# Optimization experiments

Hardware: AMD Instinct MI355X
Metric: run time of the kernel (lower is better)

The kernel has to match this reference:

```python
import jax, jax.numpy as jnp
import numpy as np

ALPHA = 0.7
MARGIN = 0.5
BATCH = 8192


def setup_inputs() -> dict:
    key = jax.random.key(0)
    k1, k2 = jax.random.split(key)
    predictions = jax.random.normal(k1, (BATCH, 1), dtype=jnp.float32)
    targets = jax.random.normal(k2, (BATCH, 1), dtype=jnp.float32)
    return {"predictions": predictions, "targets": targets}


def reference(predictions, targets):
    # MSE term (mean over all elements, as nn.MSELoss default)
    mse_loss = jnp.mean((predictions - targets) ** 2)

    p = predictions[:, 0]  # [B]
    t = targets[:, 0]      # [B]
    B = p.shape[0]

    # Pairwise differences [B, B]
    dt = t[:, None] - t[None, :]
    dp = p[:, None] - p[None, :]

    # Original loop visits ordered pairs i < j and, depending on sign(t_i - t_j),
    # computes relu(margin - sign(t_i - t_j) * (p_i - p_j)); ties are skipped.
    upper = jnp.triu(jnp.ones((B, B), dtype=bool), k=1)
    valid = upper & (dt != 0)
    pair_loss = jax.nn.relu(MARGIN - jnp.sign(dt) * dp)

    count = jnp.sum(valid)
    ranking_sum = jnp.sum(jnp.where(valid, pair_loss, 0.0))
    ranking_loss = jnp.where(count > 0, ranking_sum / jnp.maximum(count, 1), 0.0)

    return ALPHA * mse_loss + (1.0 - ALPHA) * ranking_loss
```

## Files before the change

### kernel.cpp

```cpp
#include <hip/hip_runtime.h>

#define ALPHA  0.7f
#define MARGIN 0.5f
#define TI 64
#define TJ 256
#define JR 4

__global__ __launch_bounds__(64) void pair_kernel(const float* __restrict__ p,
                                                  const float* __restrict__ t,
                                                  int B,
                                                  float* __restrict__ bsum,
                                                  float* __restrict__ bmse,
                                                  int*   __restrict__ bcnt) {
    const int bid = blockIdx.x;
    int jt = (int)((sqrtf(1.0f + 2.0f * (float)bid) - 1.0f) * 0.5f);
    while (2 * (jt + 1) * (jt + 2) <= bid) ++jt;
    while (2 * jt * (jt + 1) > bid) --jt;
    const int it  = bid - 2 * jt * (jt + 1);

    const int tid   = threadIdx.x;
    const int ig0   = it * TI;
    const int jbase = jt * TJ;
    const int j0    = jbase + tid * JR;

    __shared__ float2 s_tp[TI];
    {
        const int ig = ig0 + tid;
        float2 v;
        if (ig < B) { v.x = t[ig]; v.y = p[ig]; }
        else        { v.x = 0.0f;  v.y = 0.0f;  }
        s_tp[tid] = v;
    }
    __syncthreads();

    float tjv[JR], pjv[JR];
    bool  jvb[JR];
    if (j0 + JR <= B) {
        const float4 tv = *reinterpret_cast<const float4*>(t + j0);
        const float4 pv = *reinterpret_cast<const float4*>(p + j0);
        tjv[0] = tv.x; tjv[1] = tv.y; tjv[2] = tv.z; tjv[3] = tv.w;
        pjv[0] = pv.x; pjv[1] = pv.y; pjv[2] = pv.z; pjv[3] = pv.w;
        jvb[0] = jvb[1] = jvb[2] = jvb[3] = true;
    } else {
        #pragma unroll
        for (int k = 0; k < JR; ++k) {
            const int jg = j0 + k;
            jvb[k] = jg < B;
            tjv[k] = jvb[k] ? t[jg] : 0.0f;
            pjv[k] = jvb[k] ? p[jg] : 0.0f;
        }
    }
    unsigned long long jm[JR];
    #pragma unroll
    for (int k = 0; k < JR; ++k) jm[k] = __ballot(jvb[k]);

    float sum[JR] = {0.0f, 0.0f, 0.0f, 0.0f};
    int   cnt = 0;
    float msev = 0.0f;

    if (it == 4 * jt) {
        #pragma unroll
        for (int k = 0; k < JR; ++k) {
            const float d = pjv[k] - tjv[k];
            msev += jvb[k] ? d * d : 0.0f;
        }
    }

    if (it < 4 * jt) {
        #pragma unroll 8
        for (int ii = 0; ii < TI; ++ii) {
            const float2 itp = s_tp[ii];
            #pragma unroll
            for (int k = 0; k < JR; ++k) {
                const float dt = itp.x - tjv[k];
                const float dp = itp.y - pjv[k];
                const unsigned sg = __float_as_uint(dt) & 0x80000000u;
                const float sdp = __uint_as_float(__float_as_uint(dp) ^ sg);
                const float v = fmaxf(MARGIN - sdp, 0.0f);
                const bool val = (dt != 0.0f);
                sum[k] += val ? v : 0.0f;
                cnt += (int)__popcll(__ballot(val) & jm[k]);
            }
        }
    } else {
        int jloc[JR];
        #pragma unroll
        for (int k = 0; k < JR; ++k) jloc[k] = j0 + k - ig0;
        #pragma unroll 4
        for (int ii = 0; ii < TI; ++ii) {
            const float2 itp = s_tp[ii];
            #pragma unroll
            for (int k = 0; k < JR; ++k) {
                const float dt = itp.x - tjv[k];
                const float dp = itp.y - pjv[k];
                const unsigned sg = __float_as_uint(dt) & 0x80000000u;
                const float sdp = __uint_as_float(__float_as_uint(dp) ^ sg);
                const float v = fmaxf(MARGIN - sdp, 0.0f);
                const bool val = (dt != 0.0f) && (ii < jloc[k]);
                sum[k] += val ? v : 0.0f;
                cnt += (int)__popcll(__ballot(val) & jm[k]);
            }
        }
    }

    float stot = 0.0f;
    #pragma unroll
    for (int k = 0; k < JR; ++k) stot += jvb[k] ? sum[k] : 0.0f;
    for (int off = 32; off > 0; off >>= 1) {
        stot += __shfl_down(stot, off);
        msev += __shfl_down(msev, off);
    }
    if (tid == 0) {
        bsum[bid] = stot;
        bmse[bid] = msev;
        bcnt[bid] = cnt;
    }
}

__global__ __launch_bounds__(256) void finalize_kernel(const float* __restrict__ bsum,
                                                       const float* __restrict__ bmse,
                                                       const int*   __restrict__ bcnt,
                                                       int NB, int B,
                                                       float* __restrict__ out) {
    const int tid = threadIdx.x;
    double S = 0.0, M = 0.0;
    long long C = 0;
    for (int k = tid; k < NB; k += 256) {
        S += (double)bsum[k];
        M += (double)bmse[k];
        C += (long long)bcnt[k];
    }
    for (int off = 32; off > 0; off >>= 1) {
        S += __shfl_down(S, off);
        M += __shfl_down(M, off);
        C += __shfl_down(C, off);
    }
    __shared__ double rs[4], rm[4];
    __shared__ long long rc[4];
    const int wid = tid >> 6, lane = tid & 63;
    if (lane == 0) { rs[wid] = S; rm[wid] = M; rc[wid] = C; }
    __syncthreads();
    if (tid == 0) {
        S = rs[0] + rs[1] + rs[2] + rs[3];
        M = rm[0] + rm[1] + rm[2] + rm[3];
        C = rc[0] + rc[1] + rc[2] + rc[3];
        const double mse  = M / (double)B;
        const double rank = (C > 0) ? (S / (double)(C > 1 ? C : 1)) : 0.0;
        out[0] = (float)((double)ALPHA * mse + (double)(1.0f - ALPHA) * rank);
    }
}

extern "C" void kernel_launch(void* const* d_in, const int* in_sizes, int n_in,
                              void* d_out, int out_size, void* d_ws, size_t ws_size,
                              hipStream_t stream) {
    const float* p = (const float*)d_in[0];
    const float* t = (const float*)d_in[1];
    const int B = in_sizes[0];

    const int NJ = (B + TJ - 1) / TJ;
    const int NB = 2 * NJ * (NJ + 1);

    float* bsum = (float*)d_ws;
    float* bmse = bsum + NB;
    int*   bcnt = (int*)(bmse + NB);

    pair_kernel<<<NB, 64, 0, stream>>>(p, t, B, bsum, bmse, bcnt);
    finalize_kernel<<<1, 256, 0, stream>>>(bsum, bmse, bcnt, NB, B, (float*)d_out);
}
```

Before: 22.50 us.

## Count valid pairs analytically and read i-values from global memory with smaller i-tiles

The pair count is no longer built from a per-iteration ballot and popcount. It is computed as the number of in-range pairs minus tie pairs, and the tie correction runs only when a wave detects an equal t via __any. The shared-memory staging and barrier are removed: i-values are read straight from global memory as wave-uniform loads, and the i-tile is halved, which doubles the block count. This cuts per-pair instruction count, but adds more blocks and per-iteration global loads that depend on cache hits.

```diff
diff --git a/kernel.cpp b/kernel.cpp
--- a/kernel.cpp
+++ b/kernel.cpp
@@ -2,9 +2,9 @@
 
 #define ALPHA  0.7f
 #define MARGIN 0.5f
-#define TI 64
-#define TJ 256
-#define JR 4
+#define TI  32
+#define TJN 256
+#define JR  4
 
 __global__ __launch_bounds__(64) void pair_kernel(const float* __restrict__ p,
                                                   const float* __restrict__ t,
@@ -13,25 +13,14 @@
                                                   float* __restrict__ bmse,
                                                   int*   __restrict__ bcnt) {
     const int bid = blockIdx.x;
-    int jt = (int)((sqrtf(1.0f + 2.0f * (float)bid) - 1.0f) * 0.5f);
-    while (2 * (jt + 1) * (jt + 2) <= bid) ++jt;
-    while (2 * jt * (jt + 1) > bid) --jt;
-    const int it  = bid - 2 * jt * (jt + 1);
+    int jt = (int)((sqrtf((float)bid + 1.0f) - 1.0f) * 0.5f);
+    while (4 * (jt + 1) * (jt + 2) <= bid) ++jt;
+    while (4 * jt * (jt + 1) > bid) --jt;
+    const int it = bid - 4 * jt * (jt + 1);
 
     const int tid   = threadIdx.x;
-    const int ig0   = it * TI;
-    const int jbase = jt * TJ;
-    const int j0    = jbase + tid * JR;
-
-    __shared__ float2 s_tp[TI];
-    {
-        const int ig = ig0 + tid;
-        float2 v;
-        if (ig < B) { v.x = t[ig]; v.y = p[ig]; }
-        else        { v.x = 0.0f;  v.y = 0.0f;  }
-        s_tp[tid] = v;
-    }
-    __syncthreads();
+    const int ibase = it * TI;
+    const int j0    = jt * TJN + tid * JR;
 
     float tjv[JR], pjv[JR];
     bool  jvb[JR];
@@ -50,15 +39,13 @@
             pjv[k] = jvb[k] ? p[jg] : 0.0f;
         }
     }
-    unsigned long long jm[JR];
-    #pragma unroll
-    for (int k = 0; k < JR; ++k) jm[k] = __ballot(jvb[k]);
 
     float sum[JR] = {0.0f, 0.0f, 0.0f, 0.0f};
-    int   cnt = 0;
+    int   ceq  = 0;
+    int   cbase = 0;
     float msev = 0.0f;
 
-    if (it == 4 * jt) {
+    if (it == 0) {
         #pragma unroll
         for (int k = 0; k < JR; ++k) {
             const float d = pjv[k] - tjv[k];
@@ -66,49 +53,74 @@
         }
     }
 
-    if (it < 4 * jt) {
+    const int ilim = min(TI, B - ibase);
+
+    if (it < 8 * jt) {
         #pragma unroll 8
         for (int ii = 0; ii < TI; ++ii) {
-            const float2 itp = s_tp[ii];
+            const float ti_s = t[ibase + ii];
+            const float pi_s = p[ibase + ii];
             #pragma unroll
             for (int k = 0; k < JR; ++k) {
-                const float dt = itp.x - tjv[k];
-                const float dp = itp.y - pjv[k];
+                const float dt = ti_s - tjv[k];
+                const float dp = pi_s - pjv[k];
                 const unsigned sg = __float_as_uint(dt) & 0x80000000u;
                 const float sdp = __uint_as_float(__float_as_uint(dp) ^ sg);
                 const float v = fmaxf(MARGIN - sdp, 0.0f);
-                const bool val = (dt != 0.0f);
-                sum[k] += val ? v : 0.0f;
-                cnt += (int)__popcll(__ballot(val) & jm[k]);
+                sum[k] += v;
+                const bool eq = (dt == 0.0f);
+                if (__any(eq)) {
+                    const bool hit = eq && jvb[k];
+                    sum[k] -= hit ? v : 0.0f;
+                    ceq    += hit ? 1 : 0;
+                }
             }
         }
-    } else {
+        int nvj = 0;
+        #pragma unroll
+        for (int k = 0; k < JR; ++k) nvj += jvb[k] ? 1 : 0;
+        cbase = TI * nvj;
+    } else if (ilim > 0) {
         int jloc[JR];
         #pragma unroll
-        for (int k = 0; k < JR; ++k) jloc[k] = j0 + k - ig0;
+        for (int k = 0; k < JR; ++k) jloc[k] = j0 + k - ibase;
         #pragma unroll 4
-        for (int ii = 0; ii < TI; ++ii) {
-            const float2 itp = s_tp[ii];
+        for (int ii = 0; ii < ilim; ++ii) {
+            const float ti_s = t[ibase + ii];
+            const float pi_s = p[ibase + ii];
             #pragma unroll
             for (int k = 0; k < JR; ++k) {
-                const float dt = itp.x - tjv[k];
-                const float dp = itp.y - pjv[k];
+                const float dt = ti_s - tjv[k];
+                const float dp = pi_s - pjv[k];
                 const unsigned sg = __float_as_uint(dt) & 0x80000000u;
                 const float sdp = __uint_as_float(__float_as_uint(dp) ^ sg);
                 const float v = fmaxf(MARGIN - sdp, 0.0f);
-                const bool val = (dt != 0.0f) && (ii < jloc[k]);
-                sum[k] += val ? v : 0.0f;
-                cnt += (int)__popcll(__ballot(val) & jm[k]);
+                const bool inr = ii < jloc[k];
+                sum[k] += inr ? v : 0.0f;
+                const bool eq = (dt == 0.0f);
+                if (__any(eq)) {
+                    const bool hit = eq && inr && jvb[k];
+                    sum[k] -= hit ? v : 0.0f;
+                    ceq    += hit ? 1 : 0;
+                }
             }
+        }
+        #pragma unroll
+        for (int k = 0; k < JR; ++k) {
+            const int c = min(max(jloc[k], 0), ilim);
+            cbase += jvb[k] ? c : 0;
         }
     }
 
     float stot = 0.0f;
     #pragma unroll
     for (int k = 0; k < JR; ++k) stot += jvb[k] ? sum[k] : 0.0f;
+    int cnt = cbase - ceq;
+
     for (int off = 32; off > 0; off >>= 1) {
         stot += __shfl_down(stot, off);
         msev += __shfl_down(msev, off);
+        cnt  += __shfl_down(cnt, off);
     }
     if (tid == 0) {
         bsum[bid] = stot;
@@ -157,8 +169,8 @@
     const float* t = (const float*)d_in[1];
     const int B = in_sizes[0];
 
-    const int NJ = (B + TJ - 1) / TJ;
-    const int NB = 2 * NJ * (NJ + 1);
+    const int NJ = (B + TJN - 1) / TJN;
+    const int NB = 4 * NJ * (NJ + 1);
 
     float* bsum = (float*)d_ws;
     float* bmse = bsum + NB;
```

After: 22.08 us. About the same (-1.8%).
